# Kernel tuning notes

Hardware: AMD Instinct MI355X
Metric: run time of the kernel (lower is better)

Reference implementation:

```python
import jax, jax.numpy as jnp
import numpy as np
from jax import lax

V, E, HD, T = 100000, 256, 512, 11
H = HD // 2
B, S = 32, 512
START, STOP = 9, 10
NEG = -10000.0


def _lstm_dir(x, h0, c0, w_ih, w_hh, b_ih, b_hh):
    # x: (time, batch, in). PyTorch gate order i, f, g, o.
    def step(carry, xt):
        h, c = carry
        g = xt @ w_ih.T + b_ih + h @ w_hh.T + b_hh
        i, f, gg, o = jnp.split(g, 4, axis=-1)
        c = jax.nn.sigmoid(f) * c + jax.nn.sigmoid(i) * jnp.tanh(gg)
        h = jax.nn.sigmoid(o) * jnp.tanh(c)
        return (h, c), h
    _, hs = lax.scan(step, (h0, c0), x)
    return hs


def _features(sentence, embed, w_ih_f, w_hh_f, b_ih_f, b_hh_f,
              w_ih_b, w_hh_b, b_ih_b, b_hh_b, h0, c0, w_out, b_out):
    x = embed[sentence]  # (B, S, E)
    # Faithful to original: torch LSTM is seq-first, so it scans over axis 0 (B)
    # with 'batch' dim S (init_hidden uses sentence.shape[1]).
    hf = _lstm_dir(x, h0[0], c0[0], w_ih_f, w_hh_f, b_ih_f, b_hh_f)
    hb = _lstm_dir(x[::-1], h0[1], c0[1], w_ih_b, w_hh_b, b_ih_b, b_hh_b)[::-1]
    out = jnp.concatenate([hf, hb], axis=-1)  # (B, S, HD)
    return out @ w_out.T + b_out  # (B, S, T)


def _viterbi(feats, transitions):
    # feats: (B, S, T); CRF treats dim0 as batch, dim1 as time (as in source).
    delta0 = jnp.full((feats.shape[0], T), NEG, feats.dtype).at[:, START].set(0.0)

    def step(delta, feat_t):
        sc = transitions[None, :, :] + delta[:, None, :]  # (B, T_to, T_from)
        new = sc.max(-1) + feat_t
        return new, jnp.argmax(sc, -1)

    feats_t = jnp.moveaxis(feats[:, 1:], 1, 0)  # (S-1, B, T)
    deltaT, psis = lax.scan(step, delta0, feats_t)
    score = deltaT.max(-1)            # (B,)
    last = jnp.argmax(deltaT, -1)     # (B,)

    def back(nxt, psi_t):
        tag = jnp.take_along_axis(psi_t, nxt[:, None], axis=-1)[:, 0]
        return tag, tag

    _, earlier = lax.scan(back, last, psis, reverse=True)  # (S-1, B)
    path = jnp.concatenate([earlier, last[None, :]], axis=0).T  # (B, S)
    return score, path


def setup_inputs() -> dict:
    key = jax.random.key(0)
    ks = jax.random.split(key, 20)
    sc = 0.05
    sentence = jax.random.randint(ks[0], (B, S), 0, V)
    embed = jax.random.normal(ks[1], (V, E), jnp.float32) * sc
    w_ih_f = jax.random.normal(ks[2], (4 * H, E), jnp.float32) * sc
    w_hh_f = jax.random.normal(ks[3], (4 * H, H), jnp.float32) * sc
    b_ih_f = jax.random.normal(ks[4], (4 * H,), jnp.float32) * sc
    b_hh_f = jax.random.normal(ks[5], (4 * H,), jnp.float32) * sc
    w_ih_b = jax.random.normal(ks[6], (4 * H, E), jnp.float32) * sc
    w_hh_b = jax.random.normal(ks[7], (4 * H, H), jnp.float32) * sc
    b_ih_b = jax.random.normal(ks[8], (4 * H,), jnp.float32) * sc
    b_hh_b = jax.random.normal(ks[9], (4 * H,), jnp.float32) * sc
    h0 = jax.random.normal(ks[10], (2, S, H), jnp.float32)
    c0 = jax.random.normal(ks[11], (2, S, H), jnp.float32)
    w_out = jax.random.normal(ks[12], (T, HD), jnp.float32) * sc
    b_out = jax.random.normal(ks[13], (T,), jnp.float32) * sc
    transitions = jax.random.normal(ks[14], (T, T), jnp.float32)
    transitions = transitions.at[START, :].set(NEG).at[:, STOP].set(NEG)
    return dict(sentence=sentence, embed=embed,
                w_ih_f=w_ih_f, w_hh_f=w_hh_f, b_ih_f=b_ih_f, b_hh_f=b_hh_f,
                w_ih_b=w_ih_b, w_hh_b=w_hh_b, b_ih_b=b_ih_b, b_hh_b=b_hh_b,
                h0=h0, c0=c0, w_out=w_out, b_out=b_out, transitions=transitions)


def reference(sentence, embed, w_ih_f, w_hh_f, b_ih_f, b_hh_f,
              w_ih_b, w_hh_b, b_ih_b, b_hh_b, h0, c0, w_out, b_out, transitions):
    feats = _features(sentence, embed, w_ih_f, w_hh_f, b_ih_f, b_hh_f,
                      w_ih_b, w_hh_b, b_ih_b, b_hh_b, h0, c0, w_out, b_out)
    return _viterbi(feats, transitions)
```

## Files before the change

### kernel.cpp

```cpp
#include <hip/hip_runtime.h>
#include <math.h>


namespace {

constexpr int T_ = 11;
constexpr int HT = 256 * 512;

__device__ __forceinline__ size_t gq_off(int t, int d, int j, int q, int s) {
  return ((((size_t)(t * 2 + d) * 256 + j) * 4 + q) * 512 + s);
}

__global__ __launch_bounds__(256) void k_prep(
    const float* __restrict__ w_ih_f, const float* __restrict__ w_ih_b,
    const float* __restrict__ w_hh_f, const float* __restrict__ w_hh_b,
    const float* __restrict__ b_ih_f, const float* __restrict__ b_hh_f,
    const float* __restrict__ b_ih_b, const float* __restrict__ b_hh_b,
    const float* __restrict__ h0, const float* __restrict__ c0,
    const float* __restrict__ w_out,
    float* __restrict__ wiq, float* __restrict__ wt4, float* __restrict__ bq,
    float* __restrict__ ct, float* __restrict__ ht_f, float* __restrict__ ht_b,
    float* __restrict__ wot) {
  const int i = blockIdx.x * 256 + threadIdx.x;
  if (i < 524288) {
    int d = i >> 18, r = i & 262143, gcr = r >> 8, k = r & 255;
    int q = gcr >> 8, j = gcr & 255;
    const float* w = d ? w_ih_b : w_ih_f;
    wiq[((size_t)(d * 256 + k) * 256 + j) * 4 + q] = w[gcr * 256 + k];
  } else if (i < 1048576) {
    int i2 = i - 524288;
    int d = i2 >> 18, r = i2 & 262143, gcr = r >> 8, k = r & 255;
    int q = gcr >> 8, j = gcr & 255;
    const float* w = d ? w_hh_b : w_hh_f;
    wt4[((size_t)(d * 256 + k) * 256 + j) * 4 + q] = w[gcr * 256 + k];
  } else if (i < 1050624) {
    int r = i - 1048576;
    int d = r >> 10, x = r & 1023, j = x >> 2, q = x & 3;
    const float* bi = d ? b_ih_b : b_ih_f;
    const float* bh = d ? b_hh_b : b_hh_f;
    bq[r] = bi[q * 256 + j] + bh[q * 256 + j];
  } else if (i < 1312768) {
    int r = i - 1050624;
    int d = r >> 17, y = r & 131071, j = y >> 9, s = y & 511;
    ct[r] = c0[((size_t)d * 512 + s) * 256 + j];
  } else if (i < 1574912) {
    int r = i - 1312768;
    int d = r >> 17, y = r & 131071, j = y >> 9, s = y & 511;
    float v = h0[((size_t)d * 512 + s) * 256 + j];
    if (d == 0) ht_f[y] = v; else ht_b[y] = v;
  } else if (i < 1580544) {
    int r = i - 1574912;
    int k = r / 11, tag = r - k * 11;
    wot[r] = w_out[tag * 512 + k];
  }
}

__global__ __launch_bounds__(256, 4) void k_ggemm(
    const int* __restrict__ sent, const float* __restrict__ embed,
    const float* __restrict__ wiq, const float* __restrict__ bq,
    float* __restrict__ Gq) {
  __shared__ float As[64][67];
  const int tid = threadIdx.x;
  const int bid = blockIdx.x;
  const int jg8 = bid & 7;
  const int d = (bid >> 3) & 1;
  const int rt = bid >> 4;
  const int wid = __builtin_amdgcn_readfirstlane(tid >> 6);
  const int lane = tid & 63;
  const int row0 = rt * 64;
  const int t = row0 >> 9;
  const int sb = (row0 & 511) + lane;
  const int j0 = (jg8 * 4 + wid) * 8;

  const int rr = tid & 63, eq = tid >> 6;
  const int tok = sent[row0 + rr];
  const float* erow = embed + (size_t)tok * 256 + eq * 16;

  float acc[32];
#pragma unroll
  for (int g = 0; g < 32; ++g) acc[g] = 0.f;

  const float* wbase = wiq + (size_t)d * 256 * 1024;

  for (int ci = 0; ci < 4; ++ci) {
    const int k0 = ci * 64;
    const float* ep = erow + k0;
    float4 v0 = *(const float4*)(ep);
    float4 v1 = *(const float4*)(ep + 4);
    float4 v2 = *(const float4*)(ep + 8);
    float4 v3 = *(const float4*)(ep + 12);
    const int kb = eq * 16;
    As[kb + 0][rr] = v0.x;  As[kb + 1][rr] = v0.y;  As[kb + 2][rr] = v0.z;  As[kb + 3][rr] = v0.w;
    As[kb + 4][rr] = v1.x;  As[kb + 5][rr] = v1.y;  As[kb + 6][rr] = v1.z;  As[kb + 7][rr] = v1.w;
    As[kb + 8][rr] = v2.x;  As[kb + 9][rr] = v2.y;  As[kb + 10][rr] = v2.z; As[kb + 11][rr] = v2.w;
    As[kb + 12][rr] = v3.x; As[kb + 13][rr] = v3.y; As[kb + 14][rr] = v3.z; As[kb + 15][rr] = v3.w;
    __syncthreads();
#pragma unroll 2
    for (int kk = 0; kk < 64; ++kk) {
      float a = As[kk][lane];
      const float* wp = wbase + (size_t)(k0 + kk) * 1024 + j0 * 4;
#pragma unroll
      for (int g = 0; g < 32; ++g) acc[g] = fmaf(a, wp[g], acc[g]);
    }
    __syncthreads();
  }
  const float* bp = bq + ((size_t)d * 256 + j0) * 4;
#pragma unroll
  for (int g = 0; g < 32; ++g) {
    int jj = g >> 2, q = g & 3;
    Gq[gq_off(t, d, j0 + jj, q, sb)] = acc[g] + bp[g];
  }
}

__global__ __launch_bounds__(512, 4) void k_rstep(
    const float* __restrict__ wt4, const float* __restrict__ Gq,
    float* __restrict__ ht_f, float* __restrict__ ht_b,
    float* __restrict__ ct, int t) {
  __shared__ float red[3][128][17];
  __shared__ float gb[4][16][33];
  const int tid = threadIdx.x;
  const int bid = blockIdx.x;
  const int jsl = bid & 15, d = (bid >> 4) & 1, sg = bid >> 5;
  const int kh = __builtin_amdgcn_readfirstlane(tid >> 7);
  const int sq = __builtin_amdgcn_readfirstlane((tid >> 6) & 1);
  const int rem = tid & 127;
  const int lane = tid & 63;
  const int j0 = jsl * 16;
  const int s0 = sg * 32 + sq * 16;
  const int tt = d ? 31 - t : t;

  float* htX = d ? ht_b : ht_f;
  const float* hprev = htX + (size_t)t * HT;
  const float* wp = wt4 + ((size_t)d * 256 + (size_t)kh * 64) * 1024 + j0 * 4 + lane;
  const float* hp = hprev + (size_t)kh * 64 * 512 + s0;

  float acc[16];
#pragma unroll
  for (int i = 0; i < 16; ++i) acc[i] = 0.f;

#pragma unroll 4
  for (int k = 0; k < 64; ++k) {
    const float w = wp[(size_t)k * 1024];
    const float* h = hp + (size_t)k * 512;
    float4 h0_ = *(const float4*)(h);
    float4 h1_ = *(const float4*)(h + 4);
    float4 h2_ = *(const float4*)(h + 8);
    float4 h3_ = *(const float4*)(h + 12);
    acc[0]  = fmaf(w, h0_.x, acc[0]);
    acc[1]  = fmaf(w, h0_.y, acc[1]);
    acc[2]  = fmaf(w, h0_.z, acc[2]);
    acc[3]  = fmaf(w, h0_.w, acc[3]);
    acc[4]  = fmaf(w, h1_.x, acc[4]);
    acc[5]  = fmaf(w, h1_.y, acc[5]);
    acc[6]  = fmaf(w, h1_.z, acc[6]);
    acc[7]  = fmaf(w, h1_.w, acc[7]);
    acc[8]  = fmaf(w, h2_.x, acc[8]);
    acc[9]  = fmaf(w, h2_.y, acc[9]);
    acc[10] = fmaf(w, h2_.z, acc[10]);
    acc[11] = fmaf(w, h2_.w, acc[11]);
    acc[12] = fmaf(w, h3_.x, acc[12]);
    acc[13] = fmaf(w, h3_.y, acc[13]);
    acc[14] = fmaf(w, h3_.z, acc[14]);
    acc[15] = fmaf(w, h3_.w, acc[15]);
  }

  if (kh > 0) {
#pragma unroll
    for (int i = 0; i < 16; ++i) red[kh - 1][rem][i] = acc[i];
  }
  __syncthreads();
  if (kh == 0) {
    const int jl = lane >> 2, q = lane & 3;
#pragma unroll
    for (int i = 0; i < 16; ++i) {
      float v = acc[i] + red[0][rem][i] + red[1][rem][i] + red[2][rem][i];
      gb[q][jl][sq * 16 + i] = v;
    }
  }
  __syncthreads();

  {
    const int jl2 = tid >> 5, sp = tid & 31;
    const int j = j0 + jl2;
    const int s = sg * 32 + sp;
    const float* gp = Gq + gq_off(tt, d, j, 0, s);
    float gi = gb[0][jl2][sp] + gp[0];
    float gf = gb[1][jl2][sp] + gp[512];
    float gg = gb[2][jl2][sp] + gp[1024];
    float go = gb[3][jl2][sp] + gp[1536];
    float si = 1.f / (1.f + expf(-gi));
    float sf = 1.f / (1.f + expf(-gf));
    float tg = tanhf(gg);
    float so = 1.f / (1.f + expf(-go));
    const size_t coff = ((size_t)d * 256 + j) * 512 + s;
    float cp = ct[coff];
    float cn = sf * cp + si * tg;
    float hn = so * tanhf(cn);
    ct[coff] = cn;
    htX[(size_t)(t + 1) * HT + (size_t)j * 512 + s] = hn;
  }
}

__global__ __launch_bounds__(256) void k_out(
    const float* __restrict__ ht_f, const float* __restrict__ ht_b,
    const float* __restrict__ wot, const float* __restrict__ b_out,
    float* __restrict__ featsT) {
  __shared__ float red[4][11][64];
  const int tid = threadIdx.x;
  const int bid = blockIdx.x;
  const int t = bid >> 3, stile = bid & 7;
  const int wid = __builtin_amdgcn_readfirstlane(tid >> 6);
  const int lane = tid & 63;
  const int s0 = stile * 64;
  const int kg0 = wid * 128;
  const float* src = (wid < 2)
      ? ht_f + (size_t)(t + 1) * HT + (size_t)kg0 * 512
      : ht_b + (size_t)(32 - t) * HT + (size_t)(kg0 - 256) * 512;

  float acc[11];
#pragma unroll
  for (int g = 0; g < 11; ++g) acc[g] = 0.f;
#pragma unroll 4
  for (int kk = 0; kk < 128; ++kk) {
    float a = src[(size_t)kk * 512 + s0 + lane];
    const float* wp = wot + (size_t)(kg0 + kk) * 11;
#pragma unroll
    for (int g = 0; g < 11; ++g) acc[g] = fmaf(a, wp[g], acc[g]);
  }
#pragma unroll
  for (int g = 0; g < 11; ++g) red[wid][g][lane] = acc[g];
  __syncthreads();
  if (wid == 0) {
#pragma unroll
    for (int g = 0; g < 11; ++g) {
      float v = red[0][g][lane] + red[1][g][lane] + red[2][g][lane] +
                red[3][g][lane] + b_out[g];
      featsT[(size_t)g * 16384 + t * 512 + s0 + lane] = v;
    }
  }
}

__global__ __launch_bounds__(128) void k_viterbi(const float* __restrict__ featsT,
                                                 const float* __restrict__ trans,
                                                 float* __restrict__ out) {
  __shared__ float fl[512 * T_];
  __shared__ unsigned char psiL[511 * T_];
  __shared__ unsigned char specL[121 * 47];
  __shared__ unsigned char selL[16];
  __shared__ int lastL;
  __shared__ float scoreL;
  const int b = blockIdx.x, tid = threadIdx.x;
  for (int i = tid; i < 512 * T_; i += 128) {
    int tag = i >> 9, s = i & 511;
    fl[s * T_ + tag] = featsT[(size_t)tag * 16384 + b * 512 + s];
  }
  __syncthreads();

  if (tid < 64) {
    const int lane = tid;
    const int to = (lane < T_) ? lane : 0;
    float tr[T_];
#pragma unroll
    for (int f = 0; f < T_; ++f) tr[f] = trans[to * T_ + f];
    float delta = (lane == 9) ? 0.f : -10000.f;

    for (int s = 1; s < 512; ++s) {
      float fv = fl[s * T_ + to];
      float v0 = tr[0] + __shfl(delta, 0, 64);
      float v1 = tr[1] + __shfl(delta, 1, 64);
      float v2 = tr[2] + __shfl(delta, 2, 64);
      float v3 = tr[3] + __shfl(delta, 3, 64);
      float v4 = tr[4] + __shfl(delta, 4, 64);
      float v5 = tr[5] + __shfl(delta, 5, 64);
      float v6 = tr[6] + __shfl(delta, 6, 64);
      float v7 = tr[7] + __shfl(delta, 7, 64);
      float v8 = tr[8] + __shfl(delta, 8, 64);
      float v9 = tr[9] + __shfl(delta, 9, 64);
      float v10 = tr[10] + __shfl(delta, 10, 64);
      float mA = fmaxf(fmaxf(v0, v1), v2);
      float mB = fmaxf(fmaxf(v3, v4), v5);
      float mC = fmaxf(fmaxf(v6, v7), v8);
      float mD = fmaxf(v9, v10);
      float m = fmaxf(fmaxf(mA, mB), fmaxf(mC, mD));
      delta = m + fv;
      unsigned msk = (v0 == m) ? 1u : 0u;
      msk |= (v1 == m) ? 2u : 0u;
      msk |= (v2 == m) ? 4u : 0u;
      msk |= (v3 == m) ? 8u : 0u;
      msk |= (v4 == m) ? 16u : 0u;
      msk |= (v5 == m) ? 32u : 0u;
      msk |= (v6 == m) ? 64u : 0u;
      msk |= (v7 == m) ? 128u : 0u;
      msk |= (v8 == m) ? 256u : 0u;
      msk |= (v9 == m) ? 512u : 0u;
      msk |= (v10 == m) ? 1024u : 0u;
      int am = __ffs(msk) - 1;
      if (lane < T_) psiL[(s - 1) * T_ + lane] = (unsigned char)am;
    }
    float d0 = __shfl(delta, 0, 64), d1 = __shfl(delta, 1, 64);
    float d2 = __shfl(delta, 2, 64), d3 = __shfl(delta, 3, 64);
    float d4 = __shfl(delta, 4, 64), d5 = __shfl(delta, 5, 64);
    float d6 = __shfl(delta, 6, 64), d7 = __shfl(delta, 7, 64);
    float d8 = __shfl(delta, 8, 64), d9 = __shfl(delta, 9, 64);
    float d10 = __shfl(delta, 10, 64);
    float mA = fmaxf(fmaxf(d0, d1), d2);
    float mB = fmaxf(fmaxf(d3, d4), d5);
    float mC = fmaxf(fmaxf(d6, d7), d8);
    float mD = fmaxf(d9, d10);
    float m = fmaxf(fmaxf(mA, mB), fmaxf(mC, mD));
    unsigned msk = (d0 == m) ? 1u : 0u;
    msk |= (d1 == m) ? 2u : 0u;
    msk |= (d2 == m) ? 4u : 0u;
    msk |= (d3 == m) ? 8u : 0u;
    msk |= (d4 == m) ? 16u : 0u;
    msk |= (d5 == m) ? 32u : 0u;
    msk |= (d6 == m) ? 64u : 0u;
    msk |= (d7 == m) ? 128u : 0u;
    msk |= (d8 == m) ? 256u : 0u;
    msk |= (d9 == m) ? 512u : 0u;
    msk |= (d10 == m) ? 1024u : 0u;
    int am = __ffs(msk) - 1;
    if (lane == 0) { lastL = am; scoreL = m; }
  }
  __syncthreads();

  const int last = lastL;
  if (tid < 121) {
    const int g = tid / 11, tau = tid - g * 11;
    const int khi = 510 - 47 * g;
    const int len = (g < 10) ? 47 : 41;
    int cur = tau;
    unsigned char* sp = &specL[(g * 11 + tau) * 47];
    for (int i = 0; i < len; ++i) {
      cur = psiL[(khi - i) * T_ + cur];
      sp[i] = (unsigned char)cur;
    }
  }
  __syncthreads();
  if (tid == 0) {
    int cur = last;
    for (int g = 0; g < 11; ++g) {
      selL[g] = (unsigned char)cur;
      int len = (g < 10) ? 47 : 41;
      cur = specL[(g * 11 + cur) * 47 + (len - 1)];
    }
    out[b] = scoreL;
    out[32 + (size_t)b * 512 + 511] = (float)last;
  }
  __syncthreads();
  if (tid < 121) {
    const int g = tid / 11, tau = tid - g * 11;
    if (tau == selL[g]) {
      const int khi = 510 - 47 * g;
      const int len = (g < 10) ? 47 : 41;
      float* path = out + 32 + (size_t)b * 512;
      const unsigned char* sp = &specL[(g * 11 + tau) * 47];
      for (int i = 0; i < len; ++i) path[khi - i] = (float)sp[i];
    }
  }
}

}

extern "C" void kernel_launch(void* const* d_in, const int* in_sizes, int n_in,
                              void* d_out, int out_size, void* d_ws, size_t ws_size,
                              hipStream_t stream) {
  const int* sent     = (const int*)d_in[0];
  const float* embed  = (const float*)d_in[1];
  const float* w_ih_f = (const float*)d_in[2];
  const float* w_hh_f = (const float*)d_in[3];
  const float* b_ih_f = (const float*)d_in[4];
  const float* b_hh_f = (const float*)d_in[5];
  const float* w_ih_b = (const float*)d_in[6];
  const float* w_hh_b = (const float*)d_in[7];
  const float* b_ih_b = (const float*)d_in[8];
  const float* b_hh_b = (const float*)d_in[9];
  const float* h0     = (const float*)d_in[10];
  const float* c0     = (const float*)d_in[11];
  const float* w_out  = (const float*)d_in[12];
  const float* b_out  = (const float*)d_in[13];
  const float* trans  = (const float*)d_in[14];

  float* ws = (float*)d_ws;
  float* Gq     = ws;
  float* ht_f   = Gq + 33554432;
  float* ht_b   = ht_f + 4325376;
  float* ct     = ht_b + 4325376;
  float* wiq    = ct + 262144;
  float* wt4    = wiq + 524288;
  float* bq     = wt4 + 524288;
  float* wot    = bq + 2048;
  float* featsT = wot + 5632;

  k_prep<<<6174, 256, 0, stream>>>(w_ih_f, w_ih_b, w_hh_f, w_hh_b,
                                   b_ih_f, b_hh_f, b_ih_b, b_hh_b,
                                   h0, c0, w_out,
                                   wiq, wt4, bq, ct, ht_f, ht_b, wot);
  k_ggemm<<<4096, 256, 0, stream>>>(sent, embed, wiq, bq, Gq);
  for (int t = 0; t < 32; ++t)
    k_rstep<<<512, 512, 0, stream>>>(wt4, Gq, ht_f, ht_b, ct, t);
  k_out<<<256, 256, 0, stream>>>(ht_f, ht_b, wot, b_out, featsT);
  k_viterbi<<<32, 128, 0, stream>>>(featsT, trans, (float*)d_out);
}
```

Baseline: 799.8 us.

## Split embedding gather into transposed staging kernel and restructure input GEMM

```diff
diff --git a/kernel.cpp b/kernel.cpp
--- a/kernel.cpp
+++ b/kernel.cpp
@@ -55,61 +55,89 @@
   }
 }
 
-__global__ __launch_bounds__(256, 4) void k_ggemm(
+__global__ __launch_bounds__(256) void k_gatherT(
     const int* __restrict__ sent, const float* __restrict__ embed,
-    const float* __restrict__ wiq, const float* __restrict__ bq,
-    float* __restrict__ Gq) {
-  __shared__ float As[64][67];
-  const int tid = threadIdx.x;
-  const int bid = blockIdx.x;
-  const int jg8 = bid & 7;
-  const int d = (bid >> 3) & 1;
-  const int rt = bid >> 4;
-  const int wid = __builtin_amdgcn_readfirstlane(tid >> 6);
-  const int lane = tid & 63;
-  const int row0 = rt * 64;
-  const int t = row0 >> 9;
-  const int sb = (row0 & 511) + lane;
-  const int j0 = (jg8 * 4 + wid) * 8;
-
-  const int rr = tid & 63, eq = tid >> 6;
-  const int tok = sent[row0 + rr];
-  const float* erow = embed + (size_t)tok * 256 + eq * 16;
-
-  float acc[32];
-#pragma unroll
-  for (int g = 0; g < 32; ++g) acc[g] = 0.f;
-
-  const float* wbase = wiq + (size_t)d * 256 * 1024;
-
-  for (int ci = 0; ci < 4; ++ci) {
-    const int k0 = ci * 64;
-    const float* ep = erow + k0;
+    float* __restrict__ xT) {
+  __shared__ float tile[64][65];
+  const int bid = blockIdx.x, tid = threadIdx.x;
+  const int st = bid & 7, et = (bid >> 3) & 3, t = bid >> 5;
+  {
+    const int sl = tid >> 2, eq = tid & 3;
+    const int tok = sent[t * 512 + st * 64 + sl];
+    const float* ep = embed + (size_t)tok * 256 + et * 64 + eq * 16;
     float4 v0 = *(const float4*)(ep);
     float4 v1 = *(const float4*)(ep + 4);
     float4 v2 = *(const float4*)(ep + 8);
     float4 v3 = *(const float4*)(ep + 12);
-    const int kb = eq * 16;
-    As[kb + 0][rr] = v0.x;  As[kb + 1][rr] = v0.y;  As[kb + 2][rr] = v0.z;  As[kb + 3][rr] = v0.w;
-    As[kb + 4][rr] = v1.x;  As[kb + 5][rr] = v1.y;  As[kb + 6][rr] = v1.z;  As[kb + 7][rr] = v1.w;
-    As[kb + 8][rr] = v2.x;  As[kb + 9][rr] = v2.y;  As[kb + 10][rr] = v2.z; As[kb + 11][rr] = v2.w;
-    As[kb + 12][rr] = v3.x; As[kb + 13][rr] = v3.y; As[kb + 14][rr] = v3.z; As[kb + 15][rr] = v3.w;
-    __syncthreads();
-#pragma unroll 2
-    for (int kk = 0; kk < 64; ++kk) {
-      float a = As[kk][lane];
-      const float* wp = wbase + (size_t)(k0 + kk) * 1024 + j0 * 4;
-#pragma unroll
-      for (int g = 0; g < 32; ++g) acc[g] = fmaf(a, wp[g], acc[g]);
-    }
-    __syncthreads();
-  }
-  const float* bp = bq + ((size_t)d * 256 + j0) * 4;
-#pragma unroll
-  for (int g = 0; g < 32; ++g) {
-    int jj = g >> 2, q = g & 3;
-    Gq[gq_off(t, d, j0 + jj, q, sb)] = acc[g] + bp[g];
-  }
+    const int e0 = eq * 16;
+    tile[e0 + 0][sl] = v0.x;  tile[e0 + 1][sl] = v0.y;  tile[e0 + 2][sl] = v0.z;  tile[e0 + 3][sl] = v0.w;
+    tile[e0 + 4][sl] = v1.x;  tile[e0 + 5][sl] = v1.y;  tile[e0 + 6][sl] = v1.z;  tile[e0 + 7][sl] = v1.w;
+    tile[e0 + 8][sl] = v2.x;  tile[e0 + 9][sl] = v2.y;  tile[e0 + 10][sl] = v2.z; tile[e0 + 11][sl] = v2.w;
+    tile[e0 + 12][sl] = v3.x; tile[e0 + 13][sl] = v3.y; tile[e0 + 14][sl] = v3.z; tile[e0 + 15][sl] = v3.w;
+  }
+  __syncthreads();
+  {
+    const int el = tid >> 2, sq2 = tid & 3;
+    float* op = xT + ((size_t)t * 256 + et * 64 + el) * 512 + st * 64 + sq2 * 16;
+    const float* tp = &tile[el][sq2 * 16];
+    *(float4*)(op + 0) = make_float4(tp[0], tp[1], tp[2], tp[3]);
+    *(float4*)(op + 4) = make_float4(tp[4], tp[5], tp[6], tp[7]);
+    *(float4*)(op + 8) = make_float4(tp[8], tp[9], tp[10], tp[11]);
+    *(float4*)(op + 12) = make_float4(tp[12], tp[13], tp[14], tp[15]);
+  }
+}
+
+__global__ __launch_bounds__(512, 4) void k_ggemm(
+    const float* __restrict__ xT, const float* __restrict__ wiq,
+    const float* __restrict__ bq, float* __restrict__ Gq) {
+  const int tid = threadIdx.x, bid = blockIdx.x;
+  const int sg = bid & 3, jsl = (bid >> 2) & 15;
+  const int d = (bid >> 6) & 1, t = bid >> 7;
+  const int wid = __builtin_amdgcn_readfirstlane(tid >> 6);
+  const int lane = tid & 63;
+  const int jl = lane >> 2, q = lane & 3;
+  const int j = jsl * 16 + jl;
+  const int s0 = sg * 128 + wid * 16;
+
+  const float* wp = wiq + (size_t)d * 262144 + jsl * 64 + lane;
+  const float* xp = xT + (size_t)t * 131072 + s0;
+
+  float acc[16];
+#pragma unroll
+  for (int i = 0; i < 16; ++i) acc[i] = 0.f;
+
+#pragma unroll 4
+  for (int k = 0; k < 256; ++k) {
+    const float w = wp[(size_t)k * 1024];
+    const float* h = xp + (size_t)k * 512;
+    float4 h0_ = *(const float4*)(h);
+    float4 h1_ = *(const float4*)(h + 4);
+    float4 h2_ = *(const float4*)(h + 8);
+    float4 h3_ = *(const float4*)(h + 12);
+    acc[0]  = fmaf(w, h0_.x, acc[0]);
+    acc[1]  = fmaf(w, h0_.y, acc[1]);
+    acc[2]  = fmaf(w, h0_.z, acc[2]);
+    acc[3]  = fmaf(w, h0_.w, acc[3]);
+    acc[4]  = fmaf(w, h1_.x, acc[4]);
+    acc[5]  = fmaf(w, h1_.y, acc[5]);
+    acc[6]  = fmaf(w, h1_.z, acc[6]);
+    acc[7]  = fmaf(w, h1_.w, acc[7]);
+    acc[8]  = fmaf(w, h2_.x, acc[8]);
+    acc[9]  = fmaf(w, h2_.y, acc[9]);
+    acc[10] = fmaf(w, h2_.z, acc[10]);
+    acc[11] = fmaf(w, h2_.w, acc[11]);
+    acc[12] = fmaf(w, h3_.x, acc[12]);
+    acc[13] = fmaf(w, h3_.y, acc[13]);
+    acc[14] = fmaf(w, h3_.z, acc[14]);
+    acc[15] = fmaf(w, h3_.w, acc[15]);
+  }
+
+  const float bias = bq[(size_t)d * 1024 + jsl * 64 + lane];
+  float* op = Gq + gq_off(t, d, j, q, s0);
+  *(float4*)(op + 0) = make_float4(acc[0] + bias, acc[1] + bias, acc[2] + bias, acc[3] + bias);
+  *(float4*)(op + 4) = make_float4(acc[4] + bias, acc[5] + bias, acc[6] + bias, acc[7] + bias);
+  *(float4*)(op + 8) = make_float4(acc[8] + bias, acc[9] + bias, acc[10] + bias, acc[11] + bias);
+  *(float4*)(op + 12) = make_float4(acc[12] + bias, acc[13] + bias, acc[14] + bias, acc[15] + bias);
 }
 
 __global__ __launch_bounds__(512, 4) void k_rstep(
@@ -391,12 +419,14 @@
   float* bq     = wt4 + 524288;
   float* wot    = bq + 2048;
   float* featsT = wot + 5632;
+  float* xT = ht_f + HT;
 
   k_prep<<<6174, 256, 0, stream>>>(w_ih_f, w_ih_b, w_hh_f, w_hh_b,
                                    b_ih_f, b_hh_f, b_ih_b, b_hh_b,
                                    h0, c0, w_out,
                                    wiq, wt4, bq, ct, ht_f, ht_b, wot);
-  k_ggemm<<<4096, 256, 0, stream>>>(sent, embed, wiq, bq, Gq);
+  k_gatherT<<<1024, 256, 0, stream>>>(sent, embed, xT);
+  k_ggemm<<<4096, 512, 0, stream>>>(xT, wiq, bq, Gq);
   for (int t = 0; t < 32; ++t)
     k_rstep<<<512, 512, 0, stream>>>(wt4, Gq, ht_f, ht_b, ct, t);
   k_out<<<256, 256, 0, stream>>>(ht_f, ht_b, wot, b_out, featsT);
```

Result: no change. 805.5 us (+0.7%).
